# Kernel tuning notes

Hardware: AMD Instinct MI355X
Metric: run time of the kernel (lower is better)

## Reference

```python
import jax, jax.numpy as jnp
import numpy as np

N_USERS = 50000
N_ENT = 200000
N = N_USERS + N_ENT
D = 128
E = 2_000_000
B = 8192
NCAT = 8
CATV = 1000
NNUM = 16
H = 2 * D  # n_hiddens = 2 * embed_dim


def setup_inputs() -> dict:
    key = jax.random.key(0)
    ks = jax.random.split(key, 32)
    s = 0.02
    inp = {}
    inp['entity_user_embed'] = jax.random.normal(ks[0], (N, D), jnp.float32) * s
    inp['A_vals'] = jax.random.uniform(ks[1], (E,), jnp.float32) / 8.0
    # category embedding tables; row 0 is padding -> zeros
    inp['user_cat_table'] = (jax.random.normal(ks[2], (CATV + 1, D), jnp.float32) * s).at[0].set(0.0)
    inp['item_cat_table'] = (jax.random.normal(ks[3], (CATV + 1, D), jnp.float32) * s).at[0].set(0.0)
    inp['num_W_user'] = jax.random.normal(ks[4], (D, NNUM), jnp.float32) * s
    inp['num_b_user'] = jax.random.normal(ks[5], (D,), jnp.float32) * s
    inp['num_W_item'] = jax.random.normal(ks[6], (D, NNUM), jnp.float32) * s
    inp['num_b_item'] = jax.random.normal(ks[7], (D,), jnp.float32) * s
    # MaskLinear stack: (2D->H), (H->H), (H->1); masks stacked over 2 tasks
    inp['W0'] = jax.random.normal(ks[8], (H, 2 * D), jnp.float32) * s
    inp['b0'] = jax.random.normal(ks[9], (H,), jnp.float32) * s
    inp['Mw0'] = jax.random.normal(ks[10], (2, H, 2 * D), jnp.float32)
    inp['Mb0'] = jax.random.normal(ks[11], (2, H), jnp.float32)
    inp['W1'] = jax.random.normal(ks[12], (H, H), jnp.float32) * s
    inp['b1'] = jax.random.normal(ks[13], (H,), jnp.float32) * s
    inp['Mw1'] = jax.random.normal(ks[14], (2, H, H), jnp.float32)
    inp['Mb1'] = jax.random.normal(ks[15], (2, H), jnp.float32)
    inp['W2'] = jax.random.normal(ks[16], (1, H), jnp.float32) * s
    inp['b2'] = jax.random.normal(ks[17], (1,), jnp.float32) * s
    inp['Mw2'] = jax.random.normal(ks[18], (2, 1, H), jnp.float32)
    inp['Mb2'] = jax.random.normal(ks[19], (2, 1), jnp.float32)
    inp['user_num_feats'] = jax.random.normal(ks[20], (N_USERS, NNUM), jnp.float32)
    inp['item_num_feats'] = jax.random.normal(ks[21], (N_ENT, NNUM), jnp.float32)
    inp['A_rows'] = jax.random.randint(ks[22], (E,), 0, N, jnp.int32)
    inp['A_cols'] = jax.random.randint(ks[23], (E,), 0, N, jnp.int32)
    # category ids; 0 means padding (some zeros occur naturally)
    inp['user_cat_feats'] = jax.random.randint(ks[24], (N_USERS, NCAT), 0, CATV + 1, jnp.int32)
    inp['item_cat_feats'] = jax.random.randint(ks[25], (N_ENT, NCAT), 0, CATV + 1, jnp.int32)
    inp['user_ids'] = jax.random.randint(ks[26], (B,), 0, N_USERS, jnp.int32)  # offset by N_ENT inside
    inp['item_ids'] = jax.random.randint(ks[27], (B,), 0, N_ENT, jnp.int32)
    return inp


def _mask_linear(x, W, b, Mw, Mb, task):
    # F.linear(x, W * sigmoid(mask_w[task]), b * sigmoid(mask_b[task]))
    return x @ (W * jax.nn.sigmoid(Mw[task])).T + b * jax.nn.sigmoid(Mb[task])


def _category_features(cat_ids, table):
    # padded-embedding mean over nonzero ids (get_category_features)
    emb = table[cat_ids]                               # [B, F, D] (row 0 is zeros)
    cnt = jnp.sum(cat_ids > 0, axis=-1).astype(jnp.float32)
    inv = jnp.where(cnt > 0, 1.0 / jnp.maximum(cnt, 1.0), 0.0)  # nan_to_num(1/cnt)
    return jnp.sum(emb, axis=1) * inv[:, None]          # [B, D]


def _side(all_embed, ids, cat_ids, num_feats, cat_table, num_W, num_b,
          W0, b0, Mw0, Mb0, W1, b1, Mw1, Mb1, W2, b2, Mw2, Mb2, task):
    embed = all_embed[ids]                              # [B, D]
    feat = _category_features(cat_ids, cat_table)
    feat = feat + jax.nn.relu(num_feats @ num_W.T + num_b)
    x = jnp.concatenate([embed, feat], axis=-1)         # [B, 2D]
    h = jax.nn.relu(_mask_linear(x, W0, b0, Mw0, Mb0, task))
    h = jax.nn.relu(_mask_linear(h, W1, b1, Mw1, Mb1, task))
    w = jax.nn.sigmoid(_mask_linear(h, W2, b2, Mw2, Mb2, task))  # [B, 1]
    return w * embed + (1.0 - w) * feat


def reference(entity_user_embed, A_vals, user_cat_table, item_cat_table,
              num_W_user, num_b_user, num_W_item, num_b_item,
              W0, b0, Mw0, Mb0, W1, b1, Mw1, Mb1, W2, b2, Mw2, Mb2,
              user_num_feats, item_num_feats,
              A_rows, A_cols, user_cat_feats, item_cat_feats, user_ids, item_ids):
    # sparse KGAT-style propagation: agg = A_in @ ego
    msgs = A_vals[:, None] * entity_user_embed[A_cols]           # [E, D]
    agg = jax.ops.segment_sum(msgs, A_rows, num_segments=N)       # [N, D]
    all_embed = entity_user_embed + agg

    u_ids_global = user_ids + N_ENT  # user ids live after entities in the table
    u = _side(all_embed, u_ids_global, user_cat_feats[user_ids], user_num_feats[user_ids],
              user_cat_table, num_W_user, num_b_user,
              W0, b0, Mw0, Mb0, W1, b1, Mw1, Mb1, W2, b2, Mw2, Mb2, task=0)
    i = _side(all_embed, item_ids, item_cat_feats[item_ids], item_num_feats[item_ids],
              item_cat_table, num_W_item, num_b_item,
              W0, b0, Mw0, Mb0, W1, b1, Mw1, Mb1, W2, b2, Mw2, Mb2, task=1)
    return jnp.sum(u * i, axis=-1)  # [B] CF scores
```

## Files before the change

kernel.cpp:

```cpp
#include <hip/hip_runtime.h>
#include <math.h>

#define N_USERS 50000
#define N_ENT   200000
#define NTOT    250000
#define D       128
#define E_EDGES 2000000
#define B       8192
#define NCAT    8
#define NNUM    16
#define CAP     64
#define BR      32

typedef __attribute__((ext_vector_type(4))) float f32x4;
typedef __attribute__((ext_vector_type(8))) short short8;

__device__ __forceinline__ float sigf(float x) { return 1.0f / (1.0f + expf(-x)); }

__device__ __forceinline__ short f2bf(float f) {
    unsigned u = __float_as_uint(f);
    unsigned r = (u + 0x7FFF + ((u >> 16) & 1)) >> 16;
    return (short)r;
}

__global__ __launch_bounds__(256) void init_weff_kernel(
    int* __restrict__ map, int* __restrict__ bincnt,
    const float* __restrict__ W0, const float* __restrict__ Mw0,
    const float* __restrict__ b0, const float* __restrict__ Mb0,
    const float* __restrict__ W1, const float* __restrict__ Mw1,
    const float* __restrict__ b1, const float* __restrict__ Mb1,
    const float* __restrict__ W2, const float* __restrict__ Mw2,
    const float* __restrict__ b2, const float* __restrict__ Mb2,
    short* __restrict__ W0h, short* __restrict__ W1h, float* __restrict__ w2eff,
    float* __restrict__ beff0, float* __restrict__ beff1, float* __restrict__ b2eff)
{
    int t = blockIdx.x * 256 + threadIdx.x;
    if (t < 62500) {
        ((int4*)map)[t] = make_int4(-1, -1, -1, -1);
        return;
    }
    t -= 62500;
    if (t < 4096) {
        ((int4*)bincnt)[t] = make_int4(0, 0, 0, 0);
        return;
    }
    int i = t - 4096;
    if (i < 131072) {
        W0h[i] = f2bf(W0[i & 65535] * sigf(Mw0[i]));
    } else if (i < 262144) {
        int ii = i - 131072;
        W1h[ii] = f2bf(W1[ii & 65535] * sigf(Mw1[ii]));
    } else if (i < 262656) {
        int ii = i - 262144;
        w2eff[ii] = W2[ii & 255] * sigf(Mw2[ii]);
    } else if (i < 263168) {
        int ii = i - 262656;
        beff0[ii] = b0[ii & 255] * sigf(Mb0[ii]);
    } else if (i < 263680) {
        int ii = i - 263168;
        beff1[ii] = b1[ii & 255] * sigf(Mb1[ii]);
    } else if (i < 263682) {
        int ii = i - 263680;
        b2eff[ii] = b2[0] * sigf(Mb2[ii]);
    }
}

__global__ __launch_bounds__(256) void build_map_kernel(
    const int* __restrict__ uids, const int* __restrict__ iids, int* __restrict__ map)
{
    int b = blockIdx.x * 256 + threadIdx.x;
    if (b < B) {
        atomicMax(&map[uids[b] + N_ENT], b);
        atomicMax(&map[iids[b]], B + b);
    }
}

__global__ __launch_bounds__(256) void scatter_kernel(
    const int* __restrict__ A_rows, const int* __restrict__ A_cols,
    const float* __restrict__ A_vals, const int* __restrict__ map,
    int* __restrict__ bincnt, int2* __restrict__ bins)
{
    const int e = blockIdx.x * 256 + threadIdx.x;
    if (e >= E_EDGES) return;
    const int slot = map[A_rows[e]];
    if (slot < 0) return;
    const int pos = atomicAdd(&bincnt[slot], 1);
    if (pos < CAP)
        bins[(size_t)slot * CAP + pos] = make_int2(A_cols[e], __float_as_int(A_vals[e]));
}

__global__ __launch_bounds__(256) void build_x_kernel(
    const int* __restrict__ uids, const int* __restrict__ iids,
    const int* __restrict__ u_catf, const int* __restrict__ i_catf,
    const float* __restrict__ u_numf, const float* __restrict__ i_numf,
    const float* __restrict__ u_tab, const float* __restrict__ i_tab,
    const float* __restrict__ numW_u, const float* __restrict__ numb_u,
    const float* __restrict__ numW_i, const float* __restrict__ numb_i,
    const float* __restrict__ embed, const int* __restrict__ map,
    const int* __restrict__ bincnt, const int2* __restrict__ bins,
    float* __restrict__ Xu, float* __restrict__ Xi)
{
    const int side = blockIdx.y;
    const int* ids = side ? iids : uids;
    const int* cat_feats = side ? i_catf : u_catf;
    const float* num_feats = side ? i_numf : u_numf;
    const float* cat_table = side ? i_tab : u_tab;
    const float* numW = side ? numW_i : numW_u;
    const float* numb = side ? numb_i : numb_u;
    float* Xo = side ? Xi : Xu;
    const int id_offset = side ? 0 : N_ENT;

    const int tid = threadIdx.x;
    const int lr  = tid >> 7;
    const int d   = tid & 127;
    const int b   = blockIdx.x * 2 + lr;
    const int uid = ids[b];
    const int grow = uid + id_offset;
    const int slot = map[grow];

    float ev = embed[(size_t)grow * D + d];

    const int n = min(bincnt[slot], CAP);
    const int2* bl = bins + (size_t)slot * CAP;
    float g0 = 0.f, g1 = 0.f;
    int j = 0;
    for (; j + 1 < n; j += 2) {
        const int2 c0 = bl[j], c1 = bl[j + 1];
        g0 += __int_as_float(c0.y) * embed[(size_t)c0.x * D + d];
        g1 += __int_as_float(c1.y) * embed[(size_t)c1.x * D + d];
    }
    if (j < n) {
        const int2 c0 = bl[j];
        g0 += __int_as_float(c0.y) * embed[(size_t)c0.x * D + d];
    }
    ev += g0 + g1;

    float csum = 0.f;
    int cnt = 0;
#pragma unroll
    for (int f = 0; f < NCAT; ++f) {
        const int cid = cat_feats[uid * NCAT + f];
        cnt += (cid > 0);
        csum += cat_table[(size_t)cid * D + d];
    }
    const float inv = (cnt > 0) ? (1.0f / (float)cnt) : 0.0f;

    float nacc = numb[d];
#pragma unroll
    for (int k = 0; k < NNUM; ++k)
        nacc += numW[d * NNUM + k] * num_feats[(size_t)uid * NNUM + k];

    const float feat = csum * inv + fmaxf(nacc, 0.0f);
    Xo[(size_t)b * 256 + d]       = ev;
    Xo[(size_t)b * 256 + 128 + d] = feat;
}

__global__ __launch_bounds__(256) void fused_mlp_kernel(
    const float* __restrict__ Xu, const float* __restrict__ Xi,
    const short* __restrict__ W0h, const short* __restrict__ W1h,
    const float* __restrict__ beff0, const float* __restrict__ beff1,
    const float* __restrict__ w2eff, const float* __restrict__ b2eff,
    float* __restrict__ w_u, float* __restrict__ w_i)
{
    const int side = blockIdx.y;
    const float* Xg = side ? Xi : Xu;
    float* wout = side ? w_i : w_u;
    const int b0 = blockIdx.x * BR;

    __shared__ __align__(16) short Xs[BR * 256];
    __shared__ float gsum[4][BR];

    const int tid = threadIdx.x;
    const int w   = tid >> 6;
    const int l   = tid & 63;
    const int l15 = l & 15;
    const int l4  = l >> 4;

#pragma unroll
    for (int i = 0; i < 4; ++i) {
        const int ch  = tid + i * 256;
        const int row = ch >> 5;
        const int c8  = (ch & 31) << 3;
        const float4 f0 = *(const float4*)(Xg + (size_t)(b0 + row) * 256 + c8);
        const float4 f1 = *(const float4*)(Xg + (size_t)(b0 + row) * 256 + c8 + 4);
        short8 hv;
        hv[0] = f2bf(f0.x); hv[1] = f2bf(f0.y); hv[2] = f2bf(f0.z); hv[3] = f2bf(f0.w);
        hv[4] = f2bf(f1.x); hv[5] = f2bf(f1.y); hv[6] = f2bf(f1.z); hv[7] = f2bf(f1.w);
        const int byte = row * 512 + ((c8 * 2) ^ ((row & 7) << 4));
        *(short8*)((char*)Xs + byte) = hv;
    }
    __syncthreads();

    const short* W0l = W0h + (size_t)side * 65536;
    const short* W1l = W1h + (size_t)side * 65536;
    const int cwbase = w * 64;

    f32x4 acc[2][4];
#pragma unroll
    for (int m = 0; m < 2; ++m)
#pragma unroll
        for (int n = 0; n < 4; ++n) acc[m][n] = (f32x4){0.f, 0.f, 0.f, 0.f};

#pragma unroll
    for (int ks = 0; ks < 8; ++ks) {
        short8 a[2];
#pragma unroll
        for (int m = 0; m < 2; ++m) {
            const int row = m * 16 + l15;
            const int kb  = ks * 64 + l4 * 16;
            a[m] = *(const short8*)((const char*)Xs + row * 512 + (kb ^ ((row & 7) << 4)));
        }
#pragma unroll
        for (int n = 0; n < 4; ++n) {
            const short8 bb = *(const short8*)(W0l + (size_t)(cwbase + n * 16 + l15) * 256 + ks * 32 + l4 * 8);
            acc[0][n] = __builtin_amdgcn_mfma_f32_16x16x32_bf16(a[0], bb, acc[0][n], 0, 0, 0);
            acc[1][n] = __builtin_amdgcn_mfma_f32_16x16x32_bf16(a[1], bb, acc[1][n], 0, 0, 0);
        }
    }
    __syncthreads();

#pragma unroll
    for (int n = 0; n < 4; ++n) {
        const int col = cwbase + n * 16 + l15;
        const float bia = beff0[side * 256 + col];
#pragma unroll
        for (int m = 0; m < 2; ++m)
#pragma unroll
            for (int r = 0; r < 4; ++r) {
                const float v = fmaxf(acc[m][n][r] + bia, 0.f);
                const int row = m * 16 + l4 * 4 + r;
                const int byte = row * 512 + ((col * 2) ^ ((row & 7) << 4));
                *(short*)((char*)Xs + byte) = f2bf(v);
            }
    }
    __syncthreads();

#pragma unroll
    for (int m = 0; m < 2; ++m)
#pragma unroll
        for (int n = 0; n < 4; ++n) acc[m][n] = (f32x4){0.f, 0.f, 0.f, 0.f};

#pragma unroll
    for (int ks = 0; ks < 8; ++ks) {
        short8 a[2];
#pragma unroll
        for (int m = 0; m < 2; ++m) {
            const int row = m * 16 + l15;
            const int kb  = ks * 64 + l4 * 16;
            a[m] = *(const short8*)((const char*)Xs + row * 512 + (kb ^ ((row & 7) << 4)));
        }
#pragma unroll
        for (int n = 0; n < 4; ++n) {
            const short8 bb = *(const short8*)(W1l + (size_t)(cwbase + n * 16 + l15) * 256 + ks * 32 + l4 * 8);
            acc[0][n] = __builtin_amdgcn_mfma_f32_16x16x32_bf16(a[0], bb, acc[0][n], 0, 0, 0);
            acc[1][n] = __builtin_amdgcn_mfma_f32_16x16x32_bf16(a[1], bb, acc[1][n], 0, 0, 0);
        }
    }

    float w2v[4], b1v[4];
#pragma unroll
    for (int n = 0; n < 4; ++n) {
        const int col = cwbase + n * 16 + l15;
        w2v[n] = w2eff[side * 256 + col];
        b1v[n] = beff1[side * 256 + col];
    }
#pragma unroll
    for (int m = 0; m < 2; ++m)
#pragma unroll
        for (int r = 0; r < 4; ++r) {
            float s = fmaxf(acc[m][0][r] + b1v[0], 0.f) * w2v[0]
                    + fmaxf(acc[m][1][r] + b1v[1], 0.f) * w2v[1]
                    + fmaxf(acc[m][2][r] + b1v[2], 0.f) * w2v[2]
                    + fmaxf(acc[m][3][r] + b1v[3], 0.f) * w2v[3];
            s += __shfl_xor(s, 1, 16);
            s += __shfl_xor(s, 2, 16);
            s += __shfl_xor(s, 4, 16);
            s += __shfl_xor(s, 8, 16);
            if (l15 == 0) gsum[w][m * 16 + l4 * 4 + r] = s;
        }
    __syncthreads();
    if (tid < BR) {
        const float s = gsum[0][tid] + gsum[1][tid] + gsum[2][tid] + gsum[3][tid]
                      + b2eff[side];
        wout[b0 + tid] = 1.0f / (1.0f + expf(-s));
    }
}

__global__ __launch_bounds__(256) void dot_kernel(
    const float* __restrict__ Xu, const float* __restrict__ Xi,
    const float* __restrict__ wu, const float* __restrict__ wi,
    float* __restrict__ out)
{
    const int tid = threadIdx.x;
    const int wv = tid >> 6, lane = tid & 63;
    const int b = blockIdx.x * 4 + wv;
    const float a = wu[b], c = wi[b];
    const float* xu = Xu + (size_t)b * 256;
    const float* xi = Xi + (size_t)b * 256;
    float s = 0.f;
#pragma unroll
    for (int q = 0; q < 2; ++q) {
        const int d = q * 64 + lane;
        const float u = a * xu[d] + (1.f - a) * xu[128 + d];
        const float v = c * xi[d] + (1.f - c) * xi[128 + d];
        s += u * v;
    }
#pragma unroll
    for (int off = 32; off > 0; off >>= 1) s += __shfl_xor(s, off, 64);
    if (lane == 0) out[b] = s;
}

extern "C" void kernel_launch(void* const* d_in, const int* in_sizes, int n_in,
                              void* d_out, int out_size, void* d_ws, size_t ws_size,
                              hipStream_t stream)
{
    const float* embed    = (const float*)d_in[0];
    const float* A_vals   = (const float*)d_in[1];
    const float* u_cat_tab= (const float*)d_in[2];
    const float* i_cat_tab= (const float*)d_in[3];
    const float* numW_u   = (const float*)d_in[4];
    const float* numb_u   = (const float*)d_in[5];
    const float* numW_i   = (const float*)d_in[6];
    const float* numb_i   = (const float*)d_in[7];
    const float* W0  = (const float*)d_in[8];
    const float* b0  = (const float*)d_in[9];
    const float* Mw0 = (const float*)d_in[10];
    const float* Mb0 = (const float*)d_in[11];
    const float* W1  = (const float*)d_in[12];
    const float* b1  = (const float*)d_in[13];
    const float* Mw1 = (const float*)d_in[14];
    const float* Mb1 = (const float*)d_in[15];
    const float* W2  = (const float*)d_in[16];
    const float* b2  = (const float*)d_in[17];
    const float* Mw2 = (const float*)d_in[18];
    const float* Mb2 = (const float*)d_in[19];
    const float* u_numf = (const float*)d_in[20];
    const float* i_numf = (const float*)d_in[21];
    const int* A_rows = (const int*)d_in[22];
    const int* A_cols = (const int*)d_in[23];
    const int* u_catf = (const int*)d_in[24];
    const int* i_catf = (const int*)d_in[25];
    const int* u_ids  = (const int*)d_in[26];
    const int* i_ids  = (const int*)d_in[27];
    float* out = (float*)d_out;

    char* ws = (char*)d_ws;
    size_t off = 0;
    auto alloc = [&](size_t bytes) -> void* {
        void* p = ws + off;
        off += (bytes + 255) & ~(size_t)255;
        return p;
    };
    int*   map     = (int*)  alloc((size_t)NTOT * 4);
    int*   bincnt  = (int*)  alloc((size_t)2 * B * 4);
    int2*  bins    = (int2*) alloc((size_t)2 * B * CAP * 8);
    short* W0h     = (short*)alloc((size_t)2 * 65536 * 2);
    short* W1h     = (short*)alloc((size_t)2 * 65536 * 2);
    float* w2eff   = (float*)alloc(512 * 4);
    float* beff0   = (float*)alloc(512 * 4);
    float* beff1   = (float*)alloc(512 * 4);
    float* b2eff   = (float*)alloc(2 * 4);
    float* Xu      = (float*)alloc((size_t)B * 256 * 4);
    float* Xi      = (float*)alloc((size_t)B * 256 * 4);
    float* w_u     = (float*)alloc((size_t)B * 4);
    float* w_i     = (float*)alloc((size_t)B * 4);

    init_weff_kernel<<<1291, 256, 0, stream>>>(
        map, bincnt,
        W0, Mw0, b0, Mb0, W1, Mw1, b1, Mb1, W2, Mw2, b2, Mb2,
        W0h, W1h, w2eff, beff0, beff1, b2eff);

    build_map_kernel<<<(B + 255) / 256, 256, 0, stream>>>(u_ids, i_ids, map);

    scatter_kernel<<<(E_EDGES + 255) / 256, 256, 0, stream>>>(
        A_rows, A_cols, A_vals, map, bincnt, bins);

    dim3 bxgrid(B / 2, 2);
    build_x_kernel<<<bxgrid, 256, 0, stream>>>(
        u_ids, i_ids, u_catf, i_catf, u_numf, i_numf, u_cat_tab, i_cat_tab,
        numW_u, numb_u, numW_i, numb_i, embed, map, bincnt, bins, Xu, Xi);

    dim3 mgrid(B / BR, 2);
    fused_mlp_kernel<<<mgrid, 256, 0, stream>>>(
        Xu, Xi, W0h, W1h, beff0, beff1, w2eff, b2eff, w_u, w_i);

    dot_kernel<<<B / 4, 256, 0, stream>>>(Xu, Xi, w_u, w_i, out);
}
```

Baseline: 86.04 us.

## Store intermediate features as bf16, restructure gather per wavefront, pair edges in scatter

The intermediate X buffers change from fp32 to bf16. This halves the bytes written by build_x and read by the MLP and dot kernels, and the MLP no longer converts on load. build_x now gives one wavefront per (row, side), with each lane handling two dims. The first eight neighbour gathers and the category and numeric loads are issued up front as vector loads to expose memory parallelism. The scatter kernel handles two edges per thread with a paired row load. The dot product now reads bf16 features instead of fp32, which lowers its precision.

```diff
diff --git a/kernel.cpp b/kernel.cpp
--- a/kernel.cpp
+++ b/kernel.cpp
@@ -21,6 +21,14 @@
     unsigned u = __float_as_uint(f);
     unsigned r = (u + 0x7FFF + ((u >> 16) & 1)) >> 16;
     return (short)r;
+}
+__device__ __forceinline__ unsigned pack_bf2(float lo, float hi) {
+    return ((unsigned)(unsigned short)f2bf(hi) << 16) | (unsigned short)f2bf(lo);
+}
+__device__ __forceinline__ float bf_lo(unsigned x) { return __uint_as_float(x << 16); }
+__device__ __forceinline__ float bf_hi(unsigned x) { return __uint_as_float(x & 0xFFFF0000u); }
+__device__ __forceinline__ float dot4(float4 a, float4 b) {
+    return a.x * b.x + a.y * b.y + a.z * b.z + a.w * b.w;
 }
 
 __global__ __launch_bounds__(256) void init_weff_kernel(
@@ -80,13 +88,21 @@
     const float* __restrict__ A_vals, const int* __restrict__ map,
     int* __restrict__ bincnt, int2* __restrict__ bins)
 {
-    const int e = blockIdx.x * 256 + threadIdx.x;
-    if (e >= E_EDGES) return;
-    const int slot = map[A_rows[e]];
-    if (slot < 0) return;
-    const int pos = atomicAdd(&bincnt[slot], 1);
-    if (pos < CAP)
-        bins[(size_t)slot * CAP + pos] = make_int2(A_cols[e], __float_as_int(A_vals[e]));
+    const int g = blockIdx.x * 256 + threadIdx.x;
+    if (g >= E_EDGES / 2) return;
+    const int2 rr = *(const int2*)(A_rows + 2 * g);
+    const int s0 = map[rr.x];
+    const int s1 = map[rr.y];
+    if (s0 >= 0) {
+        const int p = atomicAdd(&bincnt[s0], 1);
+        if (p < CAP)
+            bins[(size_t)s0 * CAP + p] = make_int2(A_cols[2 * g], __float_as_int(A_vals[2 * g]));
+    }
+    if (s1 >= 0) {
+        const int p = atomicAdd(&bincnt[s1], 1);
+        if (p < CAP)
+            bins[(size_t)s1 * CAP + p] = make_int2(A_cols[2 * g + 1], __float_as_int(A_vals[2 * g + 1]));
+    }
 }
 
 __global__ __launch_bounds__(256) void build_x_kernel(
@@ -98,72 +114,104 @@
     const float* __restrict__ numW_i, const float* __restrict__ numb_i,
     const float* __restrict__ embed, const int* __restrict__ map,
     const int* __restrict__ bincnt, const int2* __restrict__ bins,
-    float* __restrict__ Xu, float* __restrict__ Xi)
-{
-    const int side = blockIdx.y;
+    unsigned short* __restrict__ Xu, unsigned short* __restrict__ Xi)
+{
+    const int wid  = (blockIdx.x * 256 + threadIdx.x) >> 6;
+    const int lane = threadIdx.x & 63;
+    const int side = wid & 1;
+    const int b    = wid >> 1;
+    const int d2   = lane * 2;
+
     const int* ids = side ? iids : uids;
     const int* cat_feats = side ? i_catf : u_catf;
     const float* num_feats = side ? i_numf : u_numf;
     const float* cat_table = side ? i_tab : u_tab;
     const float* numW = side ? numW_i : numW_u;
     const float* numb = side ? numb_i : numb_u;
-    float* Xo = side ? Xi : Xu;
-    const int id_offset = side ? 0 : N_ENT;
-
-    const int tid = threadIdx.x;
-    const int lr  = tid >> 7;
-    const int d   = tid & 127;
-    const int b   = blockIdx.x * 2 + lr;
-    const int uid = ids[b];
-    const int grow = uid + id_offset;
-    const int slot = map[grow];
-
-    float ev = embed[(size_t)grow * D + d];
-
-    const int n = min(bincnt[slot], CAP);
+    unsigned short* Xo = side ? Xi : Xu;
+
+    const int uid  = __builtin_amdgcn_readfirstlane(ids[b]);
+    const int grow = uid + (side ? 0 : N_ENT);
+    const int slot = __builtin_amdgcn_readfirstlane(map[grow]);
+    const int n    = min(__builtin_amdgcn_readfirstlane(bincnt[slot]), CAP);
+
+    const float2 ev0 = *(const float2*)(embed + (size_t)grow * D + d2);
+    const int4* bl4 = (const int4*)(bins + (size_t)slot * CAP);
+    const int4 ea = bl4[0], eb = bl4[1], ec = bl4[2], ed = bl4[3];
+    const int4 cf0 = *(const int4*)(cat_feats + uid * NCAT);
+    const int4 cf1 = *(const int4*)(cat_feats + uid * NCAT + 4);
+    const float4* nf = (const float4*)(num_feats + (size_t)uid * NNUM);
+    const float4 f0 = nf[0], f1 = nf[1], f2v = nf[2], f3 = nf[3];
+    const float2 nbv = *(const float2*)(numb + d2);
+
+    float gx = 0.f, gy = 0.f;
+    {
+        int  cc[8]; float vv[8];
+        cc[0]=ea.x; vv[0]=__int_as_float(ea.y); cc[1]=ea.z; vv[1]=__int_as_float(ea.w);
+        cc[2]=eb.x; vv[2]=__int_as_float(eb.y); cc[3]=eb.z; vv[3]=__int_as_float(eb.w);
+        cc[4]=ec.x; vv[4]=__int_as_float(ec.y); cc[5]=ec.z; vv[5]=__int_as_float(ec.w);
+        cc[6]=ed.x; vv[6]=__int_as_float(ed.y); cc[7]=ed.z; vv[7]=__int_as_float(ed.w);
+        float2 r[8];
+#pragma unroll
+        for (int j = 0; j < 8; ++j) {
+            const int c = (j < n) ? cc[j] : 0;
+            r[j] = *(const float2*)(embed + (size_t)c * D + d2);
+        }
+#pragma unroll
+        for (int j = 0; j < 8; ++j) {
+            const float v = (j < n) ? vv[j] : 0.f;
+            gx += v * r[j].x;
+            gy += v * r[j].y;
+        }
+    }
     const int2* bl = bins + (size_t)slot * CAP;
-    float g0 = 0.f, g1 = 0.f;
-    int j = 0;
-    for (; j + 1 < n; j += 2) {
-        const int2 c0 = bl[j], c1 = bl[j + 1];
-        g0 += __int_as_float(c0.y) * embed[(size_t)c0.x * D + d];
-        g1 += __int_as_float(c1.y) * embed[(size_t)c1.x * D + d];
-    }
-    if (j < n) {
+    for (int j = 8; j < n; j += 2) {
         const int2 c0 = bl[j];
-        g0 += __int_as_float(c0.y) * embed[(size_t)c0.x * D + d];
-    }
-    ev += g0 + g1;
-
-    float csum = 0.f;
+        const bool has1 = (j + 1 < n);
+        const int2 c1 = has1 ? bl[j + 1] : make_int2(0, 0);
+        const float2 r0 = *(const float2*)(embed + (size_t)c0.x * D + d2);
+        const float2 r1 = *(const float2*)(embed + (size_t)c1.x * D + d2);
+        const float v0 = __int_as_float(c0.y);
+        const float v1 = has1 ? __int_as_float(c1.y) : 0.f;
+        gx += v0 * r0.x + v1 * r1.x;
+        gy += v0 * r0.y + v1 * r1.y;
+    }
+
+    int cid[8] = {cf0.x, cf0.y, cf0.z, cf0.w, cf1.x, cf1.y, cf1.z, cf1.w};
     int cnt = 0;
 #pragma unroll
-    for (int f = 0; f < NCAT; ++f) {
-        const int cid = cat_feats[uid * NCAT + f];
-        cnt += (cid > 0);
-        csum += cat_table[(size_t)cid * D + d];
-    }
+    for (int f = 0; f < 8; ++f) cnt += (cid[f] > 0);
+    float2 ct[8];
+#pragma unroll
+    for (int f = 0; f < 8; ++f)
+        ct[f] = *(const float2*)(cat_table + (size_t)cid[f] * D + d2);
+    float csx = 0.f, csy = 0.f;
+#pragma unroll
+    for (int f = 0; f < 8; ++f) { csx += ct[f].x; csy += ct[f].y; }
     const float inv = (cnt > 0) ? (1.0f / (float)cnt) : 0.0f;
 
-    float nacc = numb[d];
-#pragma unroll
-    for (int k = 0; k < NNUM; ++k)
-        nacc += numW[d * NNUM + k] * num_feats[(size_t)uid * NNUM + k];
-
-    const float feat = csum * inv + fmaxf(nacc, 0.0f);
-    Xo[(size_t)b * 256 + d]       = ev;
-    Xo[(size_t)b * 256 + 128 + d] = feat;
+    const float4* w0r = (const float4*)(numW + (size_t)d2 * NNUM);
+    const float4* w1r = (const float4*)(numW + (size_t)(d2 + 1) * NNUM);
+    float na = nbv.x + dot4(w0r[0], f0) + dot4(w0r[1], f1) + dot4(w0r[2], f2v) + dot4(w0r[3], f3);
+    float nb_ = nbv.y + dot4(w1r[0], f0) + dot4(w1r[1], f1) + dot4(w1r[2], f2v) + dot4(w1r[3], f3);
+
+    const float fx = csx * inv + fmaxf(na, 0.f);
+    const float fy = csy * inv + fmaxf(nb_, 0.f);
+
+    unsigned short* row = Xo + (size_t)b * 256;
+    *(unsigned*)(row + d2)       = pack_bf2(ev0.x + gx, ev0.y + gy);
+    *(unsigned*)(row + 128 + d2) = pack_bf2(fx, fy);
 }
 
 __global__ __launch_bounds__(256) void fused_mlp_kernel(
-    const float* __restrict__ Xu, const float* __restrict__ Xi,
+    const unsigned short* __restrict__ Xu, const unsigned short* __restrict__ Xi,
     const short* __restrict__ W0h, const short* __restrict__ W1h,
     const float* __restrict__ beff0, const float* __restrict__ beff1,
     const float* __restrict__ w2eff, const float* __restrict__ b2eff,
     float* __restrict__ w_u, float* __restrict__ w_i)
 {
     const int side = blockIdx.y;
-    const float* Xg = side ? Xi : Xu;
+    const unsigned short* Xg = side ? Xi : Xu;
     float* wout = side ? w_i : w_u;
     const int b0 = blockIdx.x * BR;
 
@@ -181,11 +229,7 @@
         const int ch  = tid + i * 256;
         const int row = ch >> 5;
         const int c8  = (ch & 31) << 3;
-        const float4 f0 = *(const float4*)(Xg + (size_t)(b0 + row) * 256 + c8);
-        const float4 f1 = *(const float4*)(Xg + (size_t)(b0 + row) * 256 + c8 + 4);
-        short8 hv;
-        hv[0] = f2bf(f0.x); hv[1] = f2bf(f0.y); hv[2] = f2bf(f0.z); hv[3] = f2bf(f0.w);
-        hv[4] = f2bf(f1.x); hv[5] = f2bf(f1.y); hv[6] = f2bf(f1.z); hv[7] = f2bf(f1.w);
+        const short8 hv = *(const short8*)(Xg + (size_t)(b0 + row) * 256 + c8);
         const int byte = row * 512 + ((c8 * 2) ^ ((row & 7) << 4));
         *(short8*)((char*)Xs + byte) = hv;
     }
@@ -287,7 +331,7 @@
 }
 
 __global__ __launch_bounds__(256) void dot_kernel(
-    const float* __restrict__ Xu, const float* __restrict__ Xi,
+    const unsigned short* __restrict__ Xu, const unsigned short* __restrict__ Xi,
     const float* __restrict__ wu, const float* __restrict__ wi,
     float* __restrict__ out)
 {
@@ -295,16 +339,17 @@
     const int wv = tid >> 6, lane = tid & 63;
     const int b = blockIdx.x * 4 + wv;
     const float a = wu[b], c = wi[b];
-    const float* xu = Xu + (size_t)b * 256;
-    const float* xi = Xi + (size_t)b * 256;
-    float s = 0.f;
-#pragma unroll
-    for (int q = 0; q < 2; ++q) {
-        const int d = q * 64 + lane;
-        const float u = a * xu[d] + (1.f - a) * xu[128 + d];
-        const float v = c * xi[d] + (1.f - c) * xi[128 + d];
-        s += u * v;
-    }
+    const unsigned short* xu = Xu + (size_t)b * 256;
+    const unsigned short* xi = Xi + (size_t)b * 256;
+    const unsigned ue = *(const unsigned*)(xu + 2 * lane);
+    const unsigned uf = *(const unsigned*)(xu + 128 + 2 * lane);
+    const unsigned ie = *(const unsigned*)(xi + 2 * lane);
+    const unsigned jf = *(const unsigned*)(xi + 128 + 2 * lane);
+    const float u0 = a * bf_lo(ue) + (1.f - a) * bf_lo(uf);
+    const float u1 = a * bf_hi(ue) + (1.f - a) * bf_hi(uf);
+    const float v0 = c * bf_lo(ie) + (1.f - c) * bf_lo(jf);
+    const float v1 = c * bf_hi(ie) + (1.f - c) * bf_hi(jf);
+    float s = u0 * v0 + u1 * v1;
 #pragma unroll
     for (int off = 32; off > 0; off >>= 1) s += __shfl_xor(s, off, 64);
     if (lane == 0) out[b] = s;
@@ -360,8 +405,8 @@
     float* beff0   = (float*)alloc(512 * 4);
     float* beff1   = (float*)alloc(512 * 4);
     float* b2eff   = (float*)alloc(2 * 4);
-    float* Xu      = (float*)alloc((size_t)B * 256 * 4);
-    float* Xi      = (float*)alloc((size_t)B * 256 * 4);
+    unsigned short* Xu = (unsigned short*)alloc((size_t)B * 256 * 2);
+    unsigned short* Xi = (unsigned short*)alloc((size_t)B * 256 * 2);
     float* w_u     = (float*)alloc((size_t)B * 4);
     float* w_i     = (float*)alloc((size_t)B * 4);
 
@@ -372,11 +417,10 @@
 
     build_map_kernel<<<(B + 255) / 256, 256, 0, stream>>>(u_ids, i_ids, map);
 
-    scatter_kernel<<<(E_EDGES + 255) / 256, 256, 0, stream>>>(
+    scatter_kernel<<<(E_EDGES / 2 + 255) / 256, 256, 0, stream>>>(
         A_rows, A_cols, A_vals, map, bincnt, bins);
 
-    dim3 bxgrid(B / 2, 2);
-    build_x_kernel<<<bxgrid, 256, 0, stream>>>(
+    build_x_kernel<<<(2 * B) / 4, 256, 0, stream>>>(
         u_ids, i_ids, u_catf, i_catf, u_numf, i_numf, u_cat_tab, i_cat_tab,
         numW_u, numb_u, numW_i, numb_i, embed, map, bincnt, bins, Xu, Xi);
 
```

Measured after the change: 83.63 us. 1.03x faster.
